# Kernel tuning notes

Measured on AMD Instinct MI355X. Metric: run time of the kernel, lower is better.

The kernel has to match this reference:

```python
import jax, jax.numpy as jnp
import numpy as np

NHEAD = 12
EPS_Z = 1e-5
EPS_LN = 1e-5


def _zscore_last(t, n):
    # torch .std is unbiased (ddof=1)
    m = t.mean(axis=-1, keepdims=True)
    var = ((t - m) ** 2).sum(axis=-1, keepdims=True) / (n - 1)
    return (t - m) / (jnp.sqrt(var) + EPS_Z)


def _layernorm(x, g, b):
    m = x.mean(axis=-1, keepdims=True)
    v = ((x - m) ** 2).mean(axis=-1, keepdims=True)
    return (x - m) * jax.lax.rsqrt(v + EPS_LN) * g + b


def setup_inputs() -> dict:
    key = jax.random.key(0)
    ks = jax.random.split(key, 20)
    B, T, D, FF, E = 2, 1024, 768, 3072, 4
    p = lambda k, shape: (jax.random.normal(k, shape, jnp.float32) * 0.02)
    return {
        "src": jax.random.normal(ks[0], (B, T, D), jnp.float32),
        "frac": jax.random.uniform(ks[1], (B, T), jnp.float32),
        "Wq": p(ks[2], (D, D)), "bq": jnp.zeros((D,), jnp.float32),
        "Wk": p(ks[3], (D, D)), "bk": jnp.zeros((D,), jnp.float32),
        "Wv": p(ks[4], (D, D)), "bv": jnp.zeros((D,), jnp.float32),
        "Wo": p(ks[5], (D, D)), "bo": jnp.zeros((D,), jnp.float32),
        "gamma": jnp.float32(1.0),
        "ln1_g": jnp.ones((D,), jnp.float32), "ln1_b": jnp.zeros((D,), jnp.float32),
        "ln2_g": jnp.ones((D,), jnp.float32), "ln2_b": jnp.zeros((D,), jnp.float32),
        "Wg": p(ks[6], (E, D)), "bg": jnp.zeros((E,), jnp.float32),
        "W1": p(ks[7], (E, D, FF)), "b1": jnp.zeros((E, FF), jnp.float32),
        "W2": p(ks[8], (E, FF, D)), "b2": jnp.zeros((E, D), jnp.float32),
    }


def reference(src, frac, Wq, bq, Wk, bk, Wv, bv, Wo, bo, gamma,
              ln1_g, ln1_b, ln2_g, ln2_b, Wg, bg, W1, b1, W2, b2):
    B, T, D = src.shape
    H = NHEAD
    hd = D // H
    scale = hd ** -0.5

    # ---- attention (add_frac_bias=False path) ----
    Q = (src @ Wq.T + bq).reshape(B, T, H, hd)
    K = (src @ Wk.T + bk).reshape(B, T, H, hd)
    V = (src @ Wv.T + bv).reshape(B, T, H, hd)
    logits = jnp.einsum('bqhd,bkhd->bhqk', Q, K) * scale
    logits = gamma * _zscore_last(logits, T)
    probs = jax.nn.softmax(logits, axis=-1)
    attn = jnp.einsum('bhqk,bkhd->bqhd', probs, V).reshape(B, T, D)
    attn = attn @ Wo.T + bo

    # ---- residual + norm1 ----
    x = _layernorm(src + attn, ln1_g, ln1_b)

    # ---- MoE top-2 feed-forward ----
    E = Wg.shape[0]
    gate_scores = jax.nn.softmax(x @ Wg.T + bg, axis=-1)          # [B,T,E]
    top2_val, top2_idx = jax.lax.top_k(gate_scores, 2)            # [B,T,2]
    combine = (jax.nn.one_hot(top2_idx, E, dtype=x.dtype)
               * top2_val[..., None]).sum(axis=-2)                # [B,T,E]
    h = jax.nn.relu(jnp.einsum('btd,edf->ebtf', x, W1) + b1[:, None, None, :])
    y = jnp.einsum('ebtf,efd->ebtd', h, W2) + b2[:, None, None, :]
    ff = jnp.einsum('ebtd,bte->btd', y, combine)

    # ---- residual + norm2 ----
    return _layernorm(x + ff, ln2_g, ln2_b)
```

## Files before the change

kernel.cpp:

```cpp
#include <hip/hip_runtime.h>

typedef unsigned short u16;
typedef short bf16x8 __attribute__((ext_vector_type(8)));
typedef float f32x4 __attribute__((ext_vector_type(4)));

#define BB 2
#define TT 1024
#define DD 768
#define HH 12
#define HD 64
#define FFD 3072
#define NE 4
#define NTOK (BB*TT)
#define CROWS 4608
#define SLABZ 3538944L

#define MFMA16(a, b, c) __builtin_amdgcn_mfma_f32_16x16x32_bf16((a), (b), (c), 0, 0, 0)

#define ASYNC16(gsrc, ldst)                                                    \
    __builtin_amdgcn_global_load_lds(                                          \
        (const __attribute__((address_space(1))) void*)(gsrc),                 \
        (__attribute__((address_space(3))) void*)(ldst), 16, 0, 0)

__device__ __forceinline__ float us2f(u16 u) {
    return __uint_as_float(((unsigned int)u) << 16);
}
__device__ __forceinline__ u16 f2us(float f) {
    unsigned int x = __float_as_uint(f);
    x += 0x7fffu + ((x >> 16) & 1u);
    return (u16)(x >> 16);
}

__global__ __launch_bounds__(256) void convert_kernel(
    const float* __restrict__ in, u16* __restrict__ out, int n8)
{
    int i = blockIdx.x * 256 + threadIdx.x;
    if (i >= n8) return;
    const float4* p = reinterpret_cast<const float4*>(in) + (size_t)i * 2;
    float4 a = p[0], b = p[1];
    u16 o[8] = {f2us(a.x), f2us(a.y), f2us(a.z), f2us(a.w),
                f2us(b.x), f2us(b.y), f2us(b.z), f2us(b.w)};
    *reinterpret_cast<uint4*>(out + (size_t)i * 8) = *reinterpret_cast<uint4*>(o);
}

__global__ __launch_bounds__(256) void transpose_convert_kernel(
    const float* __restrict__ src, u16* __restrict__ dst,
    int C, int dstStride, long srcZ, long dstZ)
{
    __shared__ float tile[32][33];
    const float* s = src + (size_t)blockIdx.z * srcZ;
    u16* d = dst + (size_t)blockIdx.z * dstZ;
    const int c0 = blockIdx.x * 32, r0 = blockIdx.y * 32;
    const int tid = threadIdx.x;
    {
        const int r = tid >> 3, cs = (tid & 7) * 4;
        float4 v = *reinterpret_cast<const float4*>(&s[(size_t)(r0 + r) * C + c0 + cs]);
        tile[r][cs] = v.x; tile[r][cs + 1] = v.y;
        tile[r][cs + 2] = v.z; tile[r][cs + 3] = v.w;
    }
    __syncthreads();
    {
        const int c = tid >> 3, rs = (tid & 7) * 4;
        u16 o[4] = {f2us(tile[rs][c]), f2us(tile[rs + 1][c]),
                    f2us(tile[rs + 2][c]), f2us(tile[rs + 3][c])};
        *reinterpret_cast<uint2*>(&d[(size_t)(c0 + c) * dstStride + r0 + rs]) =
            *reinterpret_cast<uint2*>(o);
    }
}

__global__ __launch_bounds__(256) void scan_build_kernel(
    const int* __restrict__ epack, int* __restrict__ cnt,
    int* __restrict__ rowtok, int* __restrict__ tok2row)
{
    __shared__ int sc[256][4];
    const int tid = threadIdx.x;
    for (int i = tid; i < CROWS; i += 256) rowtok[i] = 0;
    int ep[8];
    int l0 = 0, l1 = 0, l2 = 0, l3 = 0;
    #pragma unroll
    for (int i = 0; i < 8; i++) {
        const int v = epack[tid * 8 + i];
        ep[i] = v;
        const int a = v & 15, b = (v >> 4) & 15;
        l0 += (a == 0) + (b == 0);
        l1 += (a == 1) + (b == 1);
        l2 += (a == 2) + (b == 2);
        l3 += (a == 3) + (b == 3);
    }
    sc[tid][0] = l0; sc[tid][1] = l1; sc[tid][2] = l2; sc[tid][3] = l3;
    __syncthreads();
    for (int off = 1; off < 256; off <<= 1) {
        int v0 = 0, v1 = 0, v2 = 0, v3 = 0;
        if (tid >= off) {
            v0 = sc[tid - off][0]; v1 = sc[tid - off][1];
            v2 = sc[tid - off][2]; v3 = sc[tid - off][3];
        }
        __syncthreads();
        if (tid >= off) {
            sc[tid][0] += v0; sc[tid][1] += v1;
            sc[tid][2] += v2; sc[tid][3] += v3;
        }
        __syncthreads();
    }
    const int t0 = sc[255][0], t1 = sc[255][1], t2 = sc[255][2], t3 = sc[255][3];
    if (tid == 0) { cnt[0] = t0; cnt[1] = t1; cnt[2] = t2; cnt[3] = t3; }
    const int b1 = (t0 + 127) & ~127;
    const int b2 = b1 + ((t1 + 127) & ~127);
    const int b3 = b2 + ((t2 + 127) & ~127);
    int r0 = sc[tid][0] - l0;
    int r1 = b1 + sc[tid][1] - l1;
    int r2 = b2 + sc[tid][2] - l2;
    int r3 = b3 + sc[tid][3] - l3;
    #pragma unroll
    for (int i = 0; i < 8; i++) {
        const int t = tid * 8 + i;
        const int a = ep[i] & 15, b = (ep[i] >> 4) & 15;
        const int ra = (a == 0) ? r0++ : (a == 1) ? r1++ : (a == 2) ? r2++ : r3++;
        rowtok[ra] = t; tok2row[t * 2] = ra;
        const int rb = (b == 0) ? r0++ : (b == 1) ? r1++ : (b == 2) ? r2++ : r3++;
        rowtok[rb] = t; tok2row[t * 2 + 1] = rb;
    }
}

__global__ __launch_bounds__(256) void gemm_bt_kernel(
    const u16* __restrict__ A, int lda, long aZ,
    const u16* __restrict__ Bt, int ldb, long bZ,
    int K, int mode, int swz,
    float* __restrict__ outF, u16* __restrict__ outH,
    u16* __restrict__ outH2, u16* __restrict__ outH3,
    int ldc, long cZ,
    const float* __restrict__ biasF, int biasZ,
    const int* __restrict__ rowtok, const int* __restrict__ cntp,
    const float* __restrict__ comb)
{
    __shared__ __align__(16) u16 As[128 * 32];
    __shared__ __align__(16) u16 Bs[128 * 32];
    const int tid = threadIdx.x;
    int bx, by, z, e = 0, baseE = 0;
    if (swz == 3) {
        const int fid = blockIdx.x;
        const int xcd = fid & 7; int r = fid >> 3;
        const int half = (r >= 96) ? 1 : 0; r -= half * 96;
        bx = r % 6; by = r / 6;
        const int ez = xcd * 2 + half; e = ez >> 2; z = ez & 3;
    } else if (swz == 1) {
        const int fid = blockIdx.x;
        const int xcd = fid & 7; const int r = fid >> 3;
        const int ne = xcd * 12 + (r % 12);
        by = r / 12; bx = ne % 24; e = ne / 24; z = e;
    } else {
        bx = blockIdx.x; by = blockIdx.y; z = blockIdx.z;
    }
    if (mode == 2 || mode == 4) {
        const int q0 = (cntp[0] + 127) & ~127;
        const int q1 = (cntp[1] + 127) & ~127;
        const int q2 = (cntp[2] + 127) & ~127;
        baseE = (e > 0 ? q0 : 0) + (e > 1 ? q1 : 0) + (e > 2 ? q2 : 0);
        if (by * 128 >= cntp[e]) return;
    }
    const int m0 = by * 128, n0 = bx * 128;
    const u16* Ab = A + (size_t)z * aZ;
    const u16* Bb = Bt + (size_t)z * bZ;
    if (mode == 4) {
        Ab += (size_t)baseE * lda;
        Bb += (size_t)e * ((size_t)DD * FFD);
    }

    const int wave = tid >> 6, lane = tid & 63;
    const int wm = (wave & 1) * 64, wn = (wave >> 1) * 64;
    const int fm = lane & 15;
    const int g  = lane >> 4;

    const int lrow = lane >> 2;
    const int lgrp = lane & 3;
    const int cg   = (lgrp ^ ((lrow >> 1) & 3)) * 8;
    const int r0   = wave * 32 + lrow;
    const u16 *aG0, *aG1;
    if (mode == 2) {
        const int t0 = rowtok[baseE + m0 + r0];
        const int t1 = rowtok[baseE + m0 + r0 + 16];
        aG0 = Ab + (size_t)t0 * lda + cg;
        aG1 = Ab + (size_t)t1 * lda + cg;
    } else {
        aG0 = Ab + (size_t)(m0 + r0) * lda + cg;
        aG1 = Ab + (size_t)(m0 + r0 + 16) * lda + cg;
    }
    const u16* bG0 = Bb + (size_t)(n0 + r0) * ldb + cg;
    const u16* bG1 = Bb + (size_t)(n0 + r0 + 16) * ldb + cg;
    u16* aL0 = &As[(wave * 32) * 32];
    u16* aL1 = &As[(wave * 32 + 16) * 32];
    u16* bL0 = &Bs[(wave * 32) * 32];
    u16* bL1 = &Bs[(wave * 32 + 16) * 32];

    const int sw8 = ((fm >> 1) & 3) * 8;
    const u16* pa[4]; const u16* pb[4];
    #pragma unroll
    for (int i = 0; i < 4; i++) {
        pa[i] = &As[(wm + i * 16 + fm) * 32 + ((g * 8) ^ sw8)];
        pb[i] = &Bs[(wn + i * 16 + fm) * 32 + ((g * 8) ^ sw8)];
    }

    f32x4 acc[4][4] = {};

    for (int k0 = 0; k0 < K; k0 += 32) {
        ASYNC16(aG0 + k0, aL0);
        ASYNC16(aG1 + k0, aL1);
        ASYNC16(bG0 + k0, bL0);
        ASYNC16(bG1 + k0, bL1);
        __syncthreads();

        bf16x8 af[4], bf[4];
        #pragma unroll
        for (int i = 0; i < 4; i++) af[i] = *reinterpret_cast<const bf16x8*>(pa[i]);
        #pragma unroll
        for (int j = 0; j < 4; j++) bf[j] = *reinterpret_cast<const bf16x8*>(pb[j]);
        #pragma unroll
        for (int i = 0; i < 4; i++)
            #pragma unroll
            for (int j = 0; j < 4; j++)
                acc[i][j] = MFMA16(af[i], bf[j], acc[i][j]);
        __syncthreads();
    }

    const int cn = lane & 15, cr = (lane >> 4) * 4;

    if (mode == 2) {
        u16* Cs = As;
        #pragma unroll
        for (int i = 0; i < 4; i++) {
            if (i) __syncthreads();
            int tokr[4]; float combr[4];
            #pragma unroll
            for (int r = 0; r < 4; r++)
                tokr[r] = rowtok[baseE + m0 + wm + i * 16 + cr + r];
            #pragma unroll
            for (int r = 0; r < 4; r++)
                combr[r] = comb[(size_t)tokr[r] * NE + z];
            #pragma unroll
            for (int j = 0; j < 4; j++) {
                const int n = n0 + wn + j * 16 + cn;
                const float bias = biasF[(size_t)z * biasZ + n];
                #pragma unroll
                for (int r = 0; r < 4; r++) {
                    float y = fmaxf(acc[i][j][r] + bias, 0.f) * combr[r];
                    Cs[((wave & 1) * 16 + cr + r) * 128 + wn + j * 16 + cn] = f2us(y);
                }
            }
            __syncthreads();
            const int lr2 = tid >> 3, c2 = (tid & 7) * 16;
            const int m2 = m0 + (lr2 >> 4) * 64 + i * 16 + (lr2 & 15);
            u16* dst = outH + (size_t)(baseE + m2) * ldc + n0 + c2;
            *reinterpret_cast<uint4*>(dst) =
                *reinterpret_cast<const uint4*>(&Cs[lr2 * 128 + c2]);
            *reinterpret_cast<uint4*>(dst + 8) =
                *reinterpret_cast<const uint4*>(&Cs[lr2 * 128 + c2 + 8]);
        }
        return;
    }

    #pragma unroll
    for (int i = 0; i < 4; i++) {
        #pragma unroll
        for (int j = 0; j < 4; j++) {
            const int n = n0 + wn + j * 16 + cn;
            #pragma unroll
            for (int r = 0; r < 4; r++) {
                const int m = m0 + wm + i * 16 + cr + r;
                float y = acc[i][j][r];
                if (mode == 0) {
                    y += biasF[n];
                    int which = (n >= 1536) ? 2 : (n >= 768 ? 1 : 0);
                    int nn = n - which * 768;
                    int bb = m >> 10, t = m & 1023;
                    int hh = nn >> 6, d = nn & 63;
                    if (which == 0)
                        outH[(((size_t)(bb * HH + hh) * TT + t) << 6) + d] = f2us(y);
                    else if (which == 1)
                        outH2[(((size_t)(bb * HH + hh) * TT + t) << 6) + d] = f2us(y);
                    else
                        outH3[(((size_t)(bb * HH + hh) * HD + d) << 10) + t] = f2us(y);
                } else {
                    float* basep = outF + (size_t)z * cZ;
                    basep[(size_t)(baseE + m) * ldc + n] = y;
                }
            }
        }
    }
}

#define PSTR 1032
__global__ __launch_bounds__(256, 2) void attn_mfma_kernel(
    const u16* __restrict__ Qh, const u16* __restrict__ Kh,
    const u16* __restrict__ VT, const float* __restrict__ gamma_p,
    u16* __restrict__ attn_out)
{
    __shared__ __align__(16) u16 P[32 * PSTR];
    __shared__ float wred[4][32][4];
    __shared__ float dred[4][32];
    __shared__ float aArr[32], cmArr[32], dinvArr[32];

    const int qt = blockIdx.x, bh = blockIdx.y;
    const int b = bh / HH, h = bh - b * HH;
    const int tid = threadIdx.x, wave = tid >> 6, lane = tid & 63;
    const int g = lane >> 4, fm = lane & 15;
    const float gamma = gamma_p[0];
    const int m0 = qt * 32;
    const u16* Qp = Qh + (size_t)bh * TT * HD;
    const u16* Kp = Kh + (size_t)bh * TT * HD;
    const u16* Vp = VT + (size_t)bh * HD * TT;

    bf16x8 af[2][2];
    #pragma unroll
    for (int mi = 0; mi < 2; mi++)
        #pragma unroll
        for (int ks = 0; ks < 2; ks++)
            af[mi][ks] = *reinterpret_cast<const bf16x8*>(
                Qp + (size_t)(m0 + mi * 16 + fm) * HD + ks * 32 + g * 8);

    const int n0w = wave * 256;
    f32x4 acc[16][2] = {};
    #pragma unroll
    for (int nj = 0; nj < 16; nj++) {
        const u16* kp = Kp + (size_t)(n0w + nj * 16 + fm) * HD + g * 8;
        bf16x8 b0 = *reinterpret_cast<const bf16x8*>(kp);
        bf16x8 b1 = *reinterpret_cast<const bf16x8*>(kp + 32);
        acc[nj][0] = MFMA16(af[0][0], b0, acc[nj][0]);
        acc[nj][0] = MFMA16(af[0][1], b1, acc[nj][0]);
        acc[nj][1] = MFMA16(af[1][0], b0, acc[nj][1]);
        acc[nj][1] = MFMA16(af[1][1], b1, acc[nj][1]);
    }

    #pragma unroll
    for (int mi = 0; mi < 2; mi++) {
        #pragma unroll
        for (int r = 0; r < 4; r++) {
            float s1 = 0.f, s2 = 0.f, mx = -3.4e38f, mn = 3.4e38f;
            #pragma unroll
            for (int nj = 0; nj < 16; nj++) {
                float v = acc[nj][mi][r];
                s1 += v; s2 = fmaf(v, v, s2);
                mx = fmaxf(mx, v); mn = fminf(mn, v);
            }
            #pragma unroll
            for (int msk = 1; msk < 16; msk <<= 1) {
                s1 += __shfl_xor(s1, msk);
                s2 += __shfl_xor(s2, msk);
                mx = fmaxf(mx, __shfl_xor(mx, msk));
                mn = fminf(mn, __shfl_xor(mn, msk));
            }
            if (fm == 0) {
                int row = mi * 16 + g * 4 + r;
                wred[wave][row][0] = s1; wred[wave][row][1] = s2;
                wred[wave][row][2] = mx; wred[wave][row][3] = mn;
            }
        }
    }
    __syncthreads();
    if (tid < 32) {
        float s1 = 0.f, s2 = 0.f, mx = -3.4e38f, mn = 3.4e38f;
        #pragma unroll
        for (int w = 0; w < 4; w++) {
            s1 += wred[w][tid][0]; s2 += wred[w][tid][1];
            mx = fmaxf(mx, wred[w][tid][2]); mn = fminf(mn, wred[w][tid][3]);
        }
        float var = (s2 - s1 * s1 * (1.f / TT)) * (1.f / (TT - 1));
        var = fmaxf(var, 0.f);
        float a = gamma / (sqrtf(var) + 8e-5f);
        aArr[tid] = a;
        cmArr[tid] = (a >= 0.f) ? a * mx : a * mn;
    }
    __syncthreads();

    #pragma unroll
    for (int mi = 0; mi < 2; mi++) {
        #pragma unroll
        for (int r = 0; r < 4; r++) {
            const int row = mi * 16 + g * 4 + r;
            const float a = aArr[row], cm = cmArr[row];
            float dp = 0.f;
            #pragma unroll
            for (int nj = 0; nj < 16; nj++) {
                float p = __expf(fmaf(a, acc[nj][mi][r], -cm));
                u16 pb = f2us(p);
                dp += us2f(pb);
                P[row * PSTR + n0w + nj * 16 + fm] = pb;
            }
            #pragma unroll
            for (int msk = 1; msk < 16; msk <<= 1) dp += __shfl_xor(dp, msk);
            if (fm == 0) dred[wave][row] = dp;
        }
    }
    __syncthreads();
    if (tid < 32)
        dinvArr[tid] = 1.f / (dred[0][tid] + dred[1][tid] + dred[2][tid] + dred[3][tid]);
    __syncthreads();

    f32x4 oacc[2] = {};
    #pragma unroll 4
    for (int ks = 0; ks < 32; ks++) {
        bf16x8 bv = *reinterpret_cast<const bf16x8*>(
            Vp + (size_t)(wave * 16 + fm) * TT + ks * 32 + g * 8);
        bf16x8 a0 = *reinterpret_cast<const bf16x8*>(&P[(size_t)fm * PSTR + ks * 32 + g * 8]);
        bf16x8 a1 = *reinterpret_cast<const bf16x8*>(&P[(size_t)(16 + fm) * PSTR + ks * 32 + g * 8]);
        oacc[0] = MFMA16(a0, bv, oacc[0]);
        oacc[1] = MFMA16(a1, bv, oacc[1]);
    }
    #pragma unroll
    for (int mi = 0; mi < 2; mi++) {
        #pragma unroll
        for (int r = 0; r < 4; r++) {
            int row = mi * 16 + g * 4 + r;
            int t = m0 + row;
            attn_out[((size_t)(b * TT + t)) * DD + h * HD + wave * 16 + fm] =
                f2us(oacc[mi][r] * dinvArr[row]);
        }
    }
}

__global__ __launch_bounds__(256) void ln1_kernel(
    const float* __restrict__ p0, const float* __restrict__ p1,
    const float* __restrict__ p2, const float* __restrict__ p3,
    const float* __restrict__ src, const float* __restrict__ bo,
    const float* __restrict__ g, const float* __restrict__ bta,
    const float* __restrict__ Wg, const float* __restrict__ bg,
    float* __restrict__ outF, u16* __restrict__ outH,
    float* __restrict__ comb, int* __restrict__ epack)
{
    const int row = blockIdx.x, tid = threadIdx.x;
    __shared__ float red[256];
    __shared__ float gred[4][4];
    const size_t base = (size_t)row * DD;
    float v[3];
    #pragma unroll
    for (int i = 0; i < 3; i++) {
        int c = tid + i * 256;
        v[i] = p0[base + c] + p1[base + c] + p2[base + c] + p3[base + c]
             + src[base + c] + bo[c];
    }
    float s = v[0] + v[1] + v[2];
    red[tid] = s; __syncthreads();
    #pragma unroll
    for (int o = 128; o > 0; o >>= 1) { if (tid < o) red[tid] += red[tid + o]; __syncthreads(); }
    const float mean = red[0] * (1.f / 768.f);
    __syncthreads();
    float qv = 0.f;
    #pragma unroll
    for (int i = 0; i < 3; i++) { float d = v[i] - mean; qv += d * d; }
    red[tid] = qv; __syncthreads();
    #pragma unroll
    for (int o = 128; o > 0; o >>= 1) { if (tid < o) red[tid] += red[tid + o]; __syncthreads(); }
    const float var = red[0] * (1.f / 768.f);
    const float rs = rsqrtf(var + 1e-5f);
    float ga0 = 0.f, ga1 = 0.f, ga2 = 0.f, ga3 = 0.f;
    #pragma unroll
    for (int i = 0; i < 3; i++) {
        int c = tid + i * 256;
        float o = (v[i] - mean) * rs * g[c] + bta[c];
        outF[base + c] = o;
        outH[base + c] = f2us(o);
        ga0 = fmaf(o, Wg[c], ga0);
        ga1 = fmaf(o, Wg[DD + c], ga1);
        ga2 = fmaf(o, Wg[2 * DD + c], ga2);
        ga3 = fmaf(o, Wg[3 * DD + c], ga3);
    }
    #pragma unroll
    for (int off = 32; off > 0; off >>= 1) {
        ga0 += __shfl_down(ga0, off, 64);
        ga1 += __shfl_down(ga1, off, 64);
        ga2 += __shfl_down(ga2, off, 64);
        ga3 += __shfl_down(ga3, off, 64);
    }
    const int wave = tid >> 6, lane = tid & 63;
    if (lane == 0) {
        gred[wave][0] = ga0; gred[wave][1] = ga1;
        gred[wave][2] = ga2; gred[wave][3] = ga3;
    }
    __syncthreads();
    if (tid == 0) {
        float gg[NE];
        #pragma unroll
        for (int e = 0; e < NE; e++)
            gg[e] = gred[0][e] + gred[1][e] + gred[2][e] + gred[3][e] + bg[e];
        float m = -1e30f;
        #pragma unroll
        for (int e = 0; e < NE; e++) m = fmaxf(m, gg[e]);
        float ex[NE], ssum = 0.f;
        #pragma unroll
        for (int e = 0; e < NE; e++) { ex[e] = __expf(gg[e] - m); ssum += ex[e]; }
        #pragma unroll
        for (int e = 0; e < NE; e++) ex[e] /= ssum;
        int e1 = 0;
        #pragma unroll
        for (int e = 1; e < NE; e++) if (ex[e] > ex[e1]) e1 = e;
        int e2 = -1;
        #pragma unroll
        for (int e = 0; e < NE; e++) if (e != e1 && (e2 < 0 || ex[e] > ex[e2])) e2 = e;
        float c[NE] = {0.f, 0.f, 0.f, 0.f};
        c[e1] = ex[e1]; c[e2] = ex[e2];
        #pragma unroll
        for (int e = 0; e < NE; e++) comb[(size_t)row * NE + e] = c[e];
        epack[row] = e1 | (e2 << 4);
    }
}

__global__ __launch_bounds__(256) void ln2_kernel(
    const float* __restrict__ x, const float* __restrict__ pslab,
    const int* __restrict__ tok2row,
    const float* __restrict__ comb, const float* __restrict__ b2,
    const float* __restrict__ g, const float* __restrict__ bta,
    float* __restrict__ outF)
{
    const int row = blockIdx.x, tid = threadIdx.x;
    __shared__ float red[256];
    const size_t base = (size_t)row * DD;
    const int r0 = tok2row[row * 2], r1 = tok2row[row * 2 + 1];
    const float* q0 = pslab + (size_t)r0 * DD;
    const float* q1 = pslab + (size_t)r1 * DD;
    const float c0 = comb[row * NE + 0], c1 = comb[row * NE + 1];
    const float c2 = comb[row * NE + 2], c3 = comb[row * NE + 3];
    float v[3];
    #pragma unroll
    for (int i = 0; i < 3; i++) {
        int c = tid + i * 256;
        float t = x[base + c];
        t += q0[c] + q0[SLABZ + c] + q0[2 * SLABZ + c] + q0[3 * SLABZ + c];
        t += q1[c] + q1[SLABZ + c] + q1[2 * SLABZ + c] + q1[3 * SLABZ + c];
        t = fmaf(c0, b2[c], t);
        t = fmaf(c1, b2[DD + c], t);
        t = fmaf(c2, b2[2 * DD + c], t);
        t = fmaf(c3, b2[3 * DD + c], t);
        v[i] = t;
    }
    float s = v[0] + v[1] + v[2];
    red[tid] = s; __syncthreads();
    #pragma unroll
    for (int o = 128; o > 0; o >>= 1) { if (tid < o) red[tid] += red[tid + o]; __syncthreads(); }
    const float mean = red[0] * (1.f / 768.f);
    __syncthreads();
    float qv = 0.f;
    #pragma unroll
    for (int i = 0; i < 3; i++) { float d = v[i] - mean; qv += d * d; }
    red[tid] = qv; __syncthreads();
    #pragma unroll
    for (int o = 128; o > 0; o >>= 1) { if (tid < o) red[tid] += red[tid + o]; __syncthreads(); }
    const float var = red[0] * (1.f / 768.f);
    const float rs = rsqrtf(var + 1e-5f);
    #pragma unroll
    for (int i = 0; i < 3; i++) {
        int c = tid + i * 256;
        outF[base + c] = (v[i] - mean) * rs * g[c] + bta[c];
    }
}

extern "C" void kernel_launch(void* const* d_in, const int* in_sizes, int n_in,
                              void* d_out, int out_size, void* d_ws, size_t ws_size,
                              hipStream_t stream)
{
    const float* src  = (const float*)d_in[0];
    const float* Wq   = (const float*)d_in[2];  const float* bq = (const float*)d_in[3];
    const float* Wk   = (const float*)d_in[4];  const float* bk = (const float*)d_in[5];
    const float* Wv   = (const float*)d_in[6];  const float* bv = (const float*)d_in[7];
    const float* Wo   = (const float*)d_in[8];  const float* bo = (const float*)d_in[9];
    const float* gam  = (const float*)d_in[10];
    const float* ln1g = (const float*)d_in[11]; const float* ln1b = (const float*)d_in[12];
    const float* ln2g = (const float*)d_in[13]; const float* ln2b = (const float*)d_in[14];
    const float* Wg   = (const float*)d_in[15]; const float* bg = (const float*)d_in[16];
    const float* W1   = (const float*)d_in[17]; const float* b1 = (const float*)d_in[18];
    const float* W2   = (const float*)d_in[19]; const float* b2 = (const float*)d_in[20];
    (void)ws_size; (void)in_sizes; (void)n_in; (void)out_size;

    char* ws = (char*)d_ws;
    u16*   W1T  = (u16*)(ws);
    float* wop  = (float*)(ws + 18874368);
    float* pslab= (float*)(ws);
    u16*   W2T  = (u16*)(ws + 56623104);
    u16*   hb   = (u16*)(ws + 75497472);
    float* x    = (float*)(ws + 103809024);
    u16*   xh   = (u16*)(ws + 110100480);
    float* comb = (float*)(ws + 113246208);
    float* bqkv = (float*)(ws + 113278976);
    int*   cnt    = (int*)(ws + 113288192);
    int*   rowtok = (int*)(ws + 113288256);
    int*   epack  = (int*)(ws + 113306688);
    int*   tok2row= (int*)(ws + 113323072);
    char* H = ws + 75497472;
    u16*   Qh     = (u16*)(H);
    u16*   Kh     = (u16*)(H + 3145728);
    u16*   VTh    = (u16*)(H + 6291456);
    u16*   src_h  = (u16*)(H + 9437184);
    u16*   attn_h = (u16*)(H + 12582912);
    u16*   WqkvH  = (u16*)(H + 15728640);
    u16*   WoH    = (u16*)(H + 19267584);
    const long PZ = (long)NTOK * DD;

    const int DW = DD * DD;

    convert_kernel<<<(NTOK * DD / 8 + 255) / 256, 256, 0, stream>>>(src, src_h, NTOK * DD / 8);
    convert_kernel<<<(DW / 8 + 255) / 256, 256, 0, stream>>>(Wq, WqkvH, DW / 8);
    convert_kernel<<<(DW / 8 + 255) / 256, 256, 0, stream>>>(Wk, WqkvH + DW, DW / 8);
    convert_kernel<<<(DW / 8 + 255) / 256, 256, 0, stream>>>(Wv, WqkvH + 2 * DW, DW / 8);
    convert_kernel<<<(DW / 8 + 255) / 256, 256, 0, stream>>>(Wo, WoH, DW / 8);
    hipMemcpyAsync(bqkv, bq, DD * 4, hipMemcpyDeviceToDevice, stream);
    hipMemcpyAsync(bqkv + DD, bk, DD * 4, hipMemcpyDeviceToDevice, stream);
    hipMemcpyAsync(bqkv + 2 * DD, bv, DD * 4, hipMemcpyDeviceToDevice, stream);
    transpose_convert_kernel<<<dim3(FFD / 32, DD / 32, NE), 256, 0, stream>>>(
        W1, W1T, FFD, DD, (long)DD * FFD, (long)FFD * DD);
    transpose_convert_kernel<<<dim3(DD / 32, FFD / 32, NE), 256, 0, stream>>>(
        W2, W2T, DD, FFD, (long)FFD * DD, (long)FFD * DD);

    gemm_bt_kernel<<<dim3(2304 / 128, NTOK / 128, 1), 256, 0, stream>>>(
        src_h, DD, 0, WqkvH, DD, 0, DD, 0, 0,
        nullptr, Qh, Kh, VTh, 0, 0, bqkv, 0, nullptr, nullptr, nullptr);

    attn_mfma_kernel<<<dim3(TT / 32, BB * HH), 256, 0, stream>>>(
        Qh, Kh, VTh, gam, attn_h);

    gemm_bt_kernel<<<dim3(DD / 128, NTOK / 128, 4), 256, 0, stream>>>(
        attn_h, DD, 192L, WoH, DD, 192L, 192, 3, 0,
        wop, nullptr, nullptr, nullptr, DD, PZ, nullptr, 0, nullptr, nullptr, nullptr);

    ln1_kernel<<<NTOK, 256, 0, stream>>>(
        wop, wop + PZ, wop + 2 * PZ, wop + 3 * PZ, src, bo,
        ln1g, ln1b, Wg, bg, x, xh, comb, epack);

    scan_build_kernel<<<1, 256, 0, stream>>>(epack, cnt, rowtok, tok2row);

    gemm_bt_kernel<<<dim3(1536, 1, 1), 256, 0, stream>>>(
        xh, DD, 0, W1T, DD, (long)FFD * DD, DD, 2, 1,
        nullptr, hb, nullptr, nullptr, FFD, 0, b1, FFD, rowtok, cnt, comb);

    gemm_bt_kernel<<<dim3(1536, 1, 1), 256, 0, stream>>>(
        hb, FFD, 768L, W2T, FFD, 768L, 768, 4, 3,
        pslab, nullptr, nullptr, nullptr, DD, SLABZ, nullptr, 0, rowtok, cnt, nullptr);

    ln2_kernel<<<NTOK, 256, 0, stream>>>(
        x, pslab, tok2row, comb, b2, ln2g, ln2b, (float*)d_out);
}
```

Measured before the change: 398.2 us.

## Double GEMM K-tile to 64 and merge conversion launches into one kernel

The bf16 GEMM now stages 64-wide K slices in LDS instead of 32, using an 8-way XOR swizzle. Each barrier pair therefore covers twice the MFMA work. Separately, five conversion launches and three bias memcpys are merged into a single kernel to cut launch overhead. The larger LDS footprint (32 KB per block) may reduce occupancy, and the K loop now assumes K is a multiple of 64. The mode-3 call uses K=192, which qualifies.

```diff
diff --git a/kernel.cpp b/kernel.cpp
--- a/kernel.cpp
+++ b/kernel.cpp
@@ -31,16 +31,36 @@
     return (u16)(x >> 16);
 }
 
-__global__ __launch_bounds__(256) void convert_kernel(
-    const float* __restrict__ in, u16* __restrict__ out, int n8)
-{
-    int i = blockIdx.x * 256 + threadIdx.x;
-    if (i >= n8) return;
-    const float4* p = reinterpret_cast<const float4*>(in) + (size_t)i * 2;
+__global__ __launch_bounds__(256) void convert5_kernel(
+    const float* __restrict__ src, const float* __restrict__ wq,
+    const float* __restrict__ wk, const float* __restrict__ wv,
+    const float* __restrict__ wo,
+    const float* __restrict__ bq, const float* __restrict__ bk,
+    const float* __restrict__ bv,
+    u16* __restrict__ src_h, u16* __restrict__ wqkv_h, u16* __restrict__ wo_h,
+    float* __restrict__ bqkv)
+{
+    const int bid = blockIdx.x, tid = threadIdx.x;
+    if (bid == 1920) {
+        for (int i = tid; i < 3 * DD; i += 256) {
+            float v = (i < DD) ? bq[i] : (i < 2 * DD) ? bk[i - DD] : bv[i - 2 * DD];
+            bqkv[i] = v;
+        }
+        return;
+    }
+    int i = bid * 256 + tid;
+    const float* in; u16* out; int off;
+    if (i < 196608) { in = src; out = src_h; off = i; }
+    else {
+        int j = i - 196608; int w = j / 73728; off = j - w * 73728;
+        in = (w == 0) ? wq : (w == 1) ? wk : (w == 2) ? wv : wo;
+        out = (w < 3) ? wqkv_h + (size_t)w * (DD * DD) : wo_h;
+    }
+    const float4* p = reinterpret_cast<const float4*>(in) + (size_t)off * 2;
     float4 a = p[0], b = p[1];
     u16 o[8] = {f2us(a.x), f2us(a.y), f2us(a.z), f2us(a.w),
                 f2us(b.x), f2us(b.y), f2us(b.z), f2us(b.w)};
-    *reinterpret_cast<uint4*>(out + (size_t)i * 8) = *reinterpret_cast<uint4*>(o);
+    *reinterpret_cast<uint4*>(out + (size_t)off * 8) = *reinterpret_cast<uint4*>(o);
 }
 
 __global__ __launch_bounds__(256) void transpose_convert_kernel(
@@ -133,8 +153,8 @@
     const int* __restrict__ rowtok, const int* __restrict__ cntp,
     const float* __restrict__ comb)
 {
-    __shared__ __align__(16) u16 As[128 * 32];
-    __shared__ __align__(16) u16 Bs[128 * 32];
+    __shared__ __align__(16) u16 As[128 * 64];
+    __shared__ __align__(16) u16 Bs[128 * 64];
     const int tid = threadIdx.x;
     int bx, by, z, e = 0, baseE = 0;
     if (swz == 3) {
@@ -171,54 +191,55 @@
     const int fm = lane & 15;
     const int g  = lane >> 4;
 
-    const int lrow = lane >> 2;
-    const int lgrp = lane & 3;
-    const int cg   = (lgrp ^ ((lrow >> 1) & 3)) * 8;
-    const int r0   = wave * 32 + lrow;
-    const u16 *aG0, *aG1;
-    if (mode == 2) {
-        const int t0 = rowtok[baseE + m0 + r0];
-        const int t1 = rowtok[baseE + m0 + r0 + 16];
-        aG0 = Ab + (size_t)t0 * lda + cg;
-        aG1 = Ab + (size_t)t1 * lda + cg;
-    } else {
-        aG0 = Ab + (size_t)(m0 + r0) * lda + cg;
-        aG1 = Ab + (size_t)(m0 + r0 + 16) * lda + cg;
-    }
-    const u16* bG0 = Bb + (size_t)(n0 + r0) * ldb + cg;
-    const u16* bG1 = Bb + (size_t)(n0 + r0 + 16) * ldb + cg;
-    u16* aL0 = &As[(wave * 32) * 32];
-    u16* aL1 = &As[(wave * 32 + 16) * 32];
-    u16* bL0 = &Bs[(wave * 32) * 32];
-    u16* bL1 = &Bs[(wave * 32 + 16) * 32];
-
-    const int sw8 = ((fm >> 1) & 3) * 8;
+    const int lr8 = lane >> 3;
+    const int cg  = ((lane & 7) ^ lr8) * 8;
+    const u16 *aG[4], *bG[4];
+    u16 *aL[4], *bL[4];
+    #pragma unroll
+    for (int i = 0; i < 4; i++) {
+        const int rr = wave * 32 + i * 8 + lr8;
+        int arow;
+        if (mode == 2) arow = rowtok[baseE + m0 + rr];
+        else           arow = m0 + rr;
+        aG[i] = Ab + (size_t)arow * lda + cg;
+        bG[i] = Bb + (size_t)(n0 + rr) * ldb + cg;
+        aL[i] = &As[(wave * 32 + i * 8) * 64];
+        bL[i] = &Bs[(wave * 32 + i * 8) * 64];
+    }
+
+    const int c0 = ((g    ) ^ (fm & 7)) * 8;
+    const int c1 = ((g + 4) ^ (fm & 7)) * 8;
     const u16* pa[4]; const u16* pb[4];
     #pragma unroll
     for (int i = 0; i < 4; i++) {
-        pa[i] = &As[(wm + i * 16 + fm) * 32 + ((g * 8) ^ sw8)];
-        pb[i] = &Bs[(wn + i * 16 + fm) * 32 + ((g * 8) ^ sw8)];
+        pa[i] = &As[(wm + i * 16 + fm) * 64];
+        pb[i] = &Bs[(wn + i * 16 + fm) * 64];
     }
 
     f32x4 acc[4][4] = {};
 
-    for (int k0 = 0; k0 < K; k0 += 32) {
-        ASYNC16(aG0 + k0, aL0);
-        ASYNC16(aG1 + k0, aL1);
-        ASYNC16(bG0 + k0, bL0);
-        ASYNC16(bG1 + k0, bL1);
+    for (int k0 = 0; k0 < K; k0 += 64) {
+        #pragma unroll
+        for (int i = 0; i < 4; i++) ASYNC16(aG[i] + k0, aL[i]);
+        #pragma unroll
+        for (int i = 0; i < 4; i++) ASYNC16(bG[i] + k0, bL[i]);
         __syncthreads();
-
-        bf16x8 af[4], bf[4];
-        #pragma unroll
-        for (int i = 0; i < 4; i++) af[i] = *reinterpret_cast<const bf16x8*>(pa[i]);
-        #pragma unroll
-        for (int j = 0; j < 4; j++) bf[j] = *reinterpret_cast<const bf16x8*>(pb[j]);
-        #pragma unroll
-        for (int i = 0; i < 4; i++)
+        #pragma unroll
+        for (int ks = 0; ks < 2; ks++) {
+            const int cc = ks ? c1 : c0;
+            bf16x8 af[4], bf[4];
+            #pragma unroll
+            for (int i = 0; i < 4; i++)
+                af[i] = *reinterpret_cast<const bf16x8*>(pa[i] + cc);
             #pragma unroll
             for (int j = 0; j < 4; j++)
-                acc[i][j] = MFMA16(af[i], bf[j], acc[i][j]);
+                bf[j] = *reinterpret_cast<const bf16x8*>(pb[j] + cc);
+            #pragma unroll
+            for (int i = 0; i < 4; i++)
+                #pragma unroll
+                for (int j = 0; j < 4; j++)
+                    acc[i][j] = MFMA16(af[i], bf[j], acc[i][j]);
+        }
         __syncthreads();
     }
 
@@ -593,16 +614,8 @@
     u16*   WoH    = (u16*)(H + 19267584);
     const long PZ = (long)NTOK * DD;
 
-    const int DW = DD * DD;
-
-    convert_kernel<<<(NTOK * DD / 8 + 255) / 256, 256, 0, stream>>>(src, src_h, NTOK * DD / 8);
-    convert_kernel<<<(DW / 8 + 255) / 256, 256, 0, stream>>>(Wq, WqkvH, DW / 8);
-    convert_kernel<<<(DW / 8 + 255) / 256, 256, 0, stream>>>(Wk, WqkvH + DW, DW / 8);
-    convert_kernel<<<(DW / 8 + 255) / 256, 256, 0, stream>>>(Wv, WqkvH + 2 * DW, DW / 8);
-    convert_kernel<<<(DW / 8 + 255) / 256, 256, 0, stream>>>(Wo, WoH, DW / 8);
-    hipMemcpyAsync(bqkv, bq, DD * 4, hipMemcpyDeviceToDevice, stream);
-    hipMemcpyAsync(bqkv + DD, bk, DD * 4, hipMemcpyDeviceToDevice, stream);
-    hipMemcpyAsync(bqkv + 2 * DD, bv, DD * 4, hipMemcpyDeviceToDevice, stream);
+    convert5_kernel<<<1921, 256, 0, stream>>>(
+        src, Wq, Wk, Wv, Wo, bq, bk, bv, src_h, WqkvH, WoH, bqkv);
     transpose_convert_kernel<<<dim3(FFD / 32, DD / 32, NE), 256, 0, stream>>>(
         W1, W1T, FFD, DD, (long)DD * FFD, (long)FFD * DD);
     transpose_convert_kernel<<<dim3(DD / 32, FFD / 32, NE), 256, 0, stream>>>(
```

Measured after the change: 369.5 us. -7.2%, faster.
